# Kernel tuning notes

Hardware: AMD Instinct MI355X
Metric: run time of the kernel (lower is better)

The kernel has to match this reference:

```python
import jax, jax.numpy as jnp
import numpy as np

N = 50000        # nodes
E = 800000       # edges (avg degree 16)
IN_DIM = 256
H = 8            # heads
D = 32           # out_dim per head
T = 4            # edge_type_num
F = 16           # edge_feature_dim
NEG_SLOPE = 0.2


def setup_inputs() -> dict:
    key = jax.random.key(0)
    ks = jax.random.split(key, 9)
    feat = jax.random.normal(ks[0], (N, IN_DIM), dtype=jnp.float32)
    e_pro = jax.random.normal(ks[1], (E, F), dtype=jnp.float32)
    mask = jax.random.uniform(ks[2], (E, T), dtype=jnp.float32)
    W_n = jax.random.normal(ks[3], (IN_DIM, H * D), dtype=jnp.float32) * (1.0 / np.sqrt(IN_DIM))
    attn_l = jax.random.normal(ks[4], (H, D, T), dtype=jnp.float32) * 0.1
    attn_r = jax.random.normal(ks[5], (H, D, T), dtype=jnp.float32) * 0.1
    attn_m = jax.random.normal(ks[6], (H, F, T), dtype=jnp.float32) * 0.1
    src = jax.random.randint(ks[7], (E,), 0, N, dtype=jnp.int32)
    dst = jax.random.randint(ks[8], (E,), 0, N, dtype=jnp.int32)
    return {"feat": feat, "e_pro": e_pro, "mask": mask, "W_n": W_n,
            "attn_l": attn_l, "attn_r": attn_r, "attn_m": attn_m,
            "src": src, "dst": dst}


def reference(feat, e_pro, mask, W_n, attn_l, attn_r, attn_m, src, dst):
    # node projection: [N, H, D]
    feat_src = (feat @ W_n).reshape(N, H, D)

    # per-node attention logits per edge type: [N, H, T]
    el = jnp.einsum("nhd,hdt->nht", feat_src, attn_l)
    er = jnp.einsum("nhd,hdt->nht", feat_src, attn_r)
    # per-edge logits per edge type: [E, H, T]
    em = jnp.einsum("ef,hft->eht", e_pro, attn_m)

    # bmm with edge-type mask [E, T] -> scalar per head: [E, H]
    left = jnp.einsum("eht,et->eh", el[src], mask)
    right = jnp.einsum("eht,et->eh", er[dst], mask)
    em_e = jnp.einsum("eht,et->eh", em, mask)

    e = (left + right + em_e) / 3.0
    e = jnp.where(e > 0, e, NEG_SLOPE * e)  # leaky_relu

    # edge softmax over incoming edges of each dst node (stable)
    e_max = jax.ops.segment_max(e, dst, num_segments=N)          # [N, H]
    e_exp = jnp.exp(e - e_max[dst])                               # [E, H]
    e_sum = jax.ops.segment_sum(e_exp, dst, num_segments=N)      # [N, H]
    a = e_exp / e_sum[dst]                                       # [E, H]

    # u_mul_e + sum aggregation: [E, H, D] -> [N, H, D]
    msg = feat_src[src] * a[:, :, None]
    rst = jax.ops.segment_sum(msg, dst, num_segments=N)

    # cat=True: concat heads
    return rst.reshape(N, H * D)
```

## Files before the change

### kernel.cpp

```cpp
#include <hip/hip_runtime.h>
#include <hip/hip_bf16.h>
#include <hip/hip_fp16.h>

#define NN 50000
#define NEDGE 800000
#define INDIM 256
#define NH 8
#define ND 32
#define HD 256
#define NT 4
#define NF 16

typedef __attribute__((ext_vector_type(8))) short s16x8;
typedef __attribute__((ext_vector_type(4))) float f32x4;
typedef unsigned short u16;

__device__ __forceinline__ float bf2f(u16 u) {
    return __uint_as_float(((unsigned int)u) << 16);
}
__device__ __forceinline__ u16 f2bf(float f) {
    __hip_bfloat16 h = __float2bfloat16(f);
    return *reinterpret_cast<u16*>(&h);
}
__device__ __forceinline__ u16 f2h(float f) {
    __half h = __float2half(f);
    return *reinterpret_cast<u16*>(&h);
}
__device__ __forceinline__ float h2f(u16 u) {
    __half h = *reinterpret_cast<__half*>(&u);
    return __half2float(h);
}

__global__ __launch_bounds__(256) void prep_kernel(const float* __restrict__ W,
                                                   u16* __restrict__ Wt,
                                                   int* __restrict__ cnt,
                                                   int* __restrict__ cursor)
{
    int idx = blockIdx.x * 256 + threadIdx.x;
    int k = idx >> 8, c = idx & 255;
    Wt[(size_t)c * 256 + k] = f2bf(W[idx]);
    if (idx < NN) { cnt[idx] = 0; cursor[idx] = 0; }
}

__global__ __launch_bounds__(256) void gemm_mfma(
    const float* __restrict__ feat, const u16* __restrict__ Wt,
    const int* __restrict__ dst, int* __restrict__ cnt,
    u16* __restrict__ fs, int nrows)
{
    const int tid = threadIdx.x;
    {
        int e0 = (blockIdx.x * 256 + tid) * 2;
        if (e0 < NEDGE)     atomicAdd(&cnt[dst[e0]], 1);
        if (e0 + 1 < NEDGE) atomicAdd(&cnt[dst[e0 + 1]], 1);
    }

    __shared__ u16 At[32 * 256];
    const int brow = blockIdx.x * 32;

    #pragma unroll
    for (int it = 0; it < 4; ++it) {
        int fo = it * 2048 + tid * 8;
        int row = fo >> 8, col = fo & 255;
        int grow = brow + row;
        if (grow >= nrows) grow = nrows - 1;
        const float* gp = feat + (size_t)grow * 256 + col;
        float4 x = *reinterpret_cast<const float4*>(gp);
        float4 y = *reinterpret_cast<const float4*>(gp + 4);
        s16x8 v;
        v[0] = (short)f2bf(x.x); v[1] = (short)f2bf(x.y);
        v[2] = (short)f2bf(x.z); v[3] = (short)f2bf(x.w);
        v[4] = (short)f2bf(y.x); v[5] = (short)f2bf(y.y);
        v[6] = (short)f2bf(y.z); v[7] = (short)f2bf(y.w);
        int byte = (col * 2) ^ ((row & 7) << 4);
        *reinterpret_cast<s16x8*>((char*)At + row * 512 + byte) = v;
    }
    __syncthreads();

    const int wave = tid >> 6, lane = tid & 63;
    const int c0 = wave * 64;
    const int rA = lane & 15;
    const int kg = lane >> 4;

    f32x4 acc[2][4] = {};

    for (int k0 = 0; k0 < 256; k0 += 32) {
        const int kk = k0 + kg * 8;
        const int byte = (kk * 2) ^ ((rA & 7) << 4);
        s16x8 a0 = *reinterpret_cast<const s16x8*>((char*)At + rA * 512 + byte);
        s16x8 a1 = *reinterpret_cast<const s16x8*>((char*)At + (16 + rA) * 512 + byte);
        #pragma unroll
        for (int ct = 0; ct < 4; ++ct) {
            s16x8 b = *reinterpret_cast<const s16x8*>(Wt + (size_t)(c0 + ct * 16 + rA) * 256 + kk);
            acc[0][ct] = __builtin_amdgcn_mfma_f32_16x16x32_bf16(a0, b, acc[0][ct], 0, 0, 0);
            acc[1][ct] = __builtin_amdgcn_mfma_f32_16x16x32_bf16(a1, b, acc[1][ct], 0, 0, 0);
        }
    }

    #pragma unroll
    for (int rt = 0; rt < 2; ++rt) {
        #pragma unroll
        for (int r = 0; r < 4; ++r) {
            int row = brow + rt * 16 + kg * 4 + r;
            if (row < nrows) {
                #pragma unroll
                for (int ct = 0; ct < 4; ++ct) {
                    fs[(size_t)row * 256 + c0 + ct * 16 + rA] = f2bf(acc[rt][ct][r]);
                }
            }
        }
    }
}

__global__ __launch_bounds__(256) void elr_kernel(
    const u16* __restrict__ fs,
    const float* __restrict__ attn_l, const float* __restrict__ attn_r,
    u16* __restrict__ el, u16* __restrict__ er, int n)
{
    __shared__ float s_al[NH * ND * NT];
    __shared__ float s_ar[NH * ND * NT];
    for (int i = threadIdx.x; i < NH * ND * NT; i += 256) {
        s_al[i] = attn_l[i];
        s_ar[i] = attn_r[i];
    }
    __syncthreads();
    int wv = threadIdx.x >> 6, lane = threadIdx.x & 63;
    int node = blockIdx.x * 4 + wv;
    if (node >= n) return;
    int h = lane >> 3, j0 = (lane & 7) * 4;
    ushort4 u = *reinterpret_cast<const ushort4*>(fs + (size_t)node * HD + lane * 4);
    float f0 = bf2f(u.x), f1 = bf2f(u.y), f2 = bf2f(u.z), f3 = bf2f(u.w);
    const float* al = s_al + h * (ND * NT) + j0 * NT;
    const float* ar = s_ar + h * (ND * NT) + j0 * NT;
    float pl[NT], pr[NT];
    #pragma unroll
    for (int t = 0; t < NT; ++t) {
        pl[t] = f0*al[t] + f1*al[NT + t] + f2*al[2*NT + t] + f3*al[3*NT + t];
        pr[t] = f0*ar[t] + f1*ar[NT + t] + f2*ar[2*NT + t] + f3*ar[3*NT + t];
    }
    #pragma unroll
    for (int d = 1; d < 8; d <<= 1) {
        #pragma unroll
        for (int t = 0; t < NT; ++t) {
            pl[t] += __shfl_xor(pl[t], d);
            pr[t] += __shfl_xor(pr[t], d);
        }
    }
    if ((lane & 7) == 0) {
        ushort4 ol, orr;
        ol.x = f2h(pl[0]); ol.y = f2h(pl[1]); ol.z = f2h(pl[2]); ol.w = f2h(pl[3]);
        orr.x = f2h(pr[0]); orr.y = f2h(pr[1]); orr.z = f2h(pr[2]); orr.w = f2h(pr[3]);
        *reinterpret_cast<ushort4*>(el + (size_t)node * (NH*NT) + h * NT) = ol;
        *reinterpret_cast<ushort4*>(er + (size_t)node * (NH*NT) + h * NT) = orr;
    }
}

__global__ void scan1_kernel(const int* __restrict__ cnt, int* __restrict__ off,
                             int* __restrict__ blksum, int n) {
    __shared__ int sm[256];
    int i = blockIdx.x * 256 + threadIdx.x;
    int v = (i < n) ? cnt[i] : 0;
    sm[threadIdx.x] = v;
    __syncthreads();
    for (int d = 1; d < 256; d <<= 1) {
        int t = (threadIdx.x >= d) ? sm[threadIdx.x - d] : 0;
        __syncthreads();
        sm[threadIdx.x] += t;
        __syncthreads();
    }
    if (i < n) off[i] = sm[threadIdx.x] - v;
    if (threadIdx.x == 255) blksum[blockIdx.x] = sm[255];
}

__global__ void scan2_kernel(int* blksum, int nb) {
    __shared__ int sm[256];
    int v = (threadIdx.x < nb) ? blksum[threadIdx.x] : 0;
    sm[threadIdx.x] = v;
    __syncthreads();
    for (int d = 1; d < 256; d <<= 1) {
        int t = (threadIdx.x >= d) ? sm[threadIdx.x - d] : 0;
        __syncthreads();
        sm[threadIdx.x] += t;
        __syncthreads();
    }
    blksum[threadIdx.x] = sm[threadIdx.x] - v;
}

__global__ void scan3_kernel(int* __restrict__ off, const int* __restrict__ blksum,
                             int n, int ne) {
    int i = blockIdx.x * 256 + threadIdx.x;
    if (i < n) off[i] += blksum[blockIdx.x];
    if (i == 0) off[n] = ne;
}

__global__ __launch_bounds__(256) void edge_kernel(
    const float* __restrict__ e_pro, const float* __restrict__ mask,
    const float* __restrict__ attn_m,
    const int* __restrict__ src, const int* __restrict__ dst,
    const u16* __restrict__ el, const u16* __restrict__ er,
    const int* __restrict__ off, int* __restrict__ cursor,
    int2* __restrict__ es, u16* __restrict__ ev, int ne)
{
    __shared__ float4 s_am4[NF][NH];
    __shared__ float s_ep[32][17];
    __shared__ float s_mk[32][5];
    const int tid = threadIdx.x;
    const int eb = blockIdx.x * 32;
    const int j = tid & 7;
    const int el_ = (tid >> 3) & 31;
    const int e = eb + (tid >> 3);

    int s = src[e], d = dst[e];
    int slot = 0;
    if (j == 0) slot = off[d] + atomicAdd(&cursor[d], 1);

    union { uint2 v; u16 u[4]; } lv, rv;
    lv.v = *reinterpret_cast<const uint2*>(el + (size_t)s * (NH*NT) + j * NT);
    rv.v = *reinterpret_cast<const uint2*>(er + (size_t)d * (NH*NT) + j * NT);

    for (int i = tid; i < NH * NF; i += 256) {
        int h = i >> 4, f = i & 15;
        const float* p = attn_m + (size_t)h * (NF * NT) + f * NT;
        s_am4[f][h] = make_float4(p[0], p[1], p[2], p[3]);
    }
    {
        int f2i = tid * 2;
        float2 v = *reinterpret_cast<const float2*>(e_pro + (size_t)eb * NF + f2i);
        int e_l = f2i >> 4, f = f2i & 15;
        s_ep[e_l][f] = v.x; s_ep[e_l][f + 1] = v.y;
    }
    if (tid < 128) {
        s_mk[tid >> 2][tid & 3] = mask[(size_t)eb * NT + tid];
    }
    __syncthreads();

    float4 mk = make_float4(s_mk[el_][0], s_mk[el_][1], s_mk[el_][2], s_mk[el_][3]);

    float em = 0.f;
    #pragma unroll
    for (int f = 0; f < NF; ++f) {
        float4 am = s_am4[f][j];
        float amm = mk.x*am.x + mk.y*am.y + mk.z*am.z + mk.w*am.w;
        em = fmaf(s_ep[el_][f], amm, em);
    }
    float left  = mk.x*h2f(lv.u[0]) + mk.y*h2f(lv.u[1]) + mk.z*h2f(lv.u[2]) + mk.w*h2f(lv.u[3]);
    float right = mk.x*h2f(rv.u[0]) + mk.y*h2f(rv.u[1]) + mk.z*h2f(rv.u[2]) + mk.w*h2f(rv.u[3]);

    float v = (left + right + em) * (1.0f / 3.0f);
    v = v > 0.f ? v : 0.2f * v;
    ev[(size_t)e * NH + j] = f2h(__expf(v));

    if (j == 0) es[slot] = make_int2(e, s);
}

__global__ __launch_bounds__(256) void agg_kernel(
    const int* __restrict__ off, const int2* __restrict__ es,
    const u16* __restrict__ ev, const u16* __restrict__ fs,
    float* __restrict__ out, int n)
{
    int wv = threadIdx.x >> 6, lane = threadIdx.x & 63;
    int node = blockIdx.x * 4 + wv;
    if (node >= n) return;
    int beg = off[node], end = off[node + 1];
    int deg = end - beg;

    int h = lane & 7, sub = lane >> 3;
    float vc[8];
    int sc[8];
    #pragma unroll
    for (int slot = 0; slot < 8; ++slot) {
        int i = beg + slot * 8 + sub;
        float v = 0.f; int sn = 0;
        if (i < end) {
            int2 p = es[i];
            v = h2f(ev[(size_t)p.x * NH + h]);
            sn = p.y;
        }
        vc[slot] = v; sc[slot] = sn;
    }

    int h2 = lane >> 3;
    const int col = lane * 4;
    float a0 = 0.f, a1 = 0.f, a2 = 0.f, a3 = 0.f, sw = 0.f;
    int deg_ = deg < 64 ? deg : 64;
    int nchunk = (deg_ + 7) >> 3;
    #pragma unroll
    for (int c = 0; c < 8; ++c) {
        if (c >= nchunk) break;
        float w8 = vc[c];
        int s8 = sc[c];
        float w[8]; int sn[8];
        #pragma unroll
        for (int q = 0; q < 8; ++q) {
            w[q]  = __shfl(w8, q * 8 + h2);
            sn[q] = __shfl(s8, q * 8 + h2);
        }
        ushort4 u[8];
        #pragma unroll
        for (int q = 0; q < 8; ++q)
            u[q] = *reinterpret_cast<const ushort4*>(fs + (size_t)sn[q] * HD + col);
        #pragma unroll
        for (int q = 0; q < 8; ++q) {
            sw += w[q];
            a0 = fmaf(w[q], bf2f(u[q].x), a0);
            a1 = fmaf(w[q], bf2f(u[q].y), a1);
            a2 = fmaf(w[q], bf2f(u[q].z), a2);
            a3 = fmaf(w[q], bf2f(u[q].w), a3);
        }
    }
    for (int i = beg + 64; i < end; ++i) {
        int2 p = es[i];
        float w = h2f(ev[(size_t)p.x * NH + h2]);
        sw += w;
        ushort4 u = *reinterpret_cast<const ushort4*>(fs + (size_t)p.y * HD + col);
        a0 = fmaf(w, bf2f(u.x), a0); a1 = fmaf(w, bf2f(u.y), a1);
        a2 = fmaf(w, bf2f(u.z), a2); a3 = fmaf(w, bf2f(u.w), a3);
    }
    float invS = sw > 0.f ? 1.f / sw : 0.f;
    a0 *= invS; a1 *= invS; a2 *= invS; a3 *= invS;
    *reinterpret_cast<float4*>(&out[(size_t)node * HD + col]) = make_float4(a0, a1, a2, a3);
}

extern "C" void kernel_launch(void* const* d_in, const int* in_sizes, int n_in,
                              void* d_out, int out_size, void* d_ws, size_t ws_size,
                              hipStream_t stream)
{
    const float* feat   = (const float*)d_in[0];
    const float* e_pro  = (const float*)d_in[1];
    const float* mask   = (const float*)d_in[2];
    const float* W_n    = (const float*)d_in[3];
    const float* attn_l = (const float*)d_in[4];
    const float* attn_r = (const float*)d_in[5];
    const float* attn_m = (const float*)d_in[6];
    const int* src      = (const int*)d_in[7];
    const int* dst      = (const int*)d_in[8];
    float* out = (float*)d_out;

    char* ws = (char*)d_ws;
    size_t o = 0;
    auto alloc = [&](size_t bytes) -> void* {
        void* p = (void*)(ws + o);
        o += (bytes + 255) & ~(size_t)255;
        return p;
    };
    u16* fs     = (u16*)alloc((size_t)NN * HD * 2);
    u16* Wt     = (u16*)alloc((size_t)INDIM * HD * 2);
    u16* el     = (u16*)alloc((size_t)NN * NH * NT * 2);
    u16* er     = (u16*)alloc((size_t)NN * NH * NT * 2);
    u16* ev     = (u16*)alloc((size_t)NEDGE * NH * 2);
    int2* es    = (int2*)alloc((size_t)NEDGE * 8);
    int* cnt    = (int*)alloc((size_t)NN * 4);
    int* cursor = (int*)alloc((size_t)NN * 4);
    int* offs   = (int*)alloc((size_t)(NN + 1) * 4);
    int* blksum = (int*)alloc(256 * 4);
    (void)ws_size; (void)in_sizes; (void)n_in; (void)out_size;

    dim3 b256(256);
    hipLaunchKernelGGL(prep_kernel, dim3(256), b256, 0, stream, W_n, Wt, cnt, cursor);
    hipLaunchKernelGGL(gemm_mfma, dim3((NN + 31) / 32), b256, 0, stream, feat, Wt, dst, cnt, fs, NN);
    hipLaunchKernelGGL(elr_kernel, dim3((NN + 3) / 4), b256, 0, stream, fs, attn_l, attn_r, el, er, NN);
    hipLaunchKernelGGL(scan1_kernel, dim3((NN + 255) / 256), b256, 0, stream, cnt, offs, blksum, NN);
    hipLaunchKernelGGL(scan2_kernel, dim3(1), b256, 0, stream, blksum, (NN + 255) / 256);
    hipLaunchKernelGGL(scan3_kernel, dim3((NN + 255) / 256), b256, 0, stream, offs, blksum, NN, NEDGE);
    hipLaunchKernelGGL(edge_kernel, dim3(NEDGE / 32), b256, 0, stream,
                       e_pro, mask, attn_m, src, dst, el, er, offs, cursor, es, ev, NEDGE);
    hipLaunchKernelGGL(agg_kernel, dim3((NN + 3) / 4), b256, 0, stream,
                       offs, es, ev, fs, out, NN);
}
```

Baseline: 232.0 us.

## Fuse edge logit computation into aggregation kernel, pack mask into CSR entries

Removes the separate edge_kernel. A light fill kernel now scatters the edge id, source and fp16-packed mask into a 16-byte CSR entry, and the aggregation kernel computes the attention logits per edge inline from e_pro, el and the per-node er. This drops the ev intermediate write and read and one wide launch. In exchange the CSR entries are twice as large, e_pro is gathered randomly (64B per edge) inside agg, and each edge's 16-feature dot product is computed in agg, which adds register pressure.

```diff
diff --git a/kernel.cpp b/kernel.cpp
--- a/kernel.cpp
+++ b/kernel.cpp
@@ -192,71 +192,35 @@
     if (i == 0) off[n] = ne;
 }
 
-__global__ __launch_bounds__(256) void edge_kernel(
-    const float* __restrict__ e_pro, const float* __restrict__ mask,
-    const float* __restrict__ attn_m,
-    const int* __restrict__ src, const int* __restrict__ dst,
-    const u16* __restrict__ el, const u16* __restrict__ er,
-    const int* __restrict__ off, int* __restrict__ cursor,
-    int2* __restrict__ es, u16* __restrict__ ev, int ne)
+__global__ void fillidx_kernel(const int* __restrict__ dst, const int* __restrict__ src,
+                               const float* __restrict__ mask,
+                               const int* __restrict__ off, int* __restrict__ cursor,
+                               int4* __restrict__ es, int ne) {
+    int e = blockIdx.x * 256 + threadIdx.x;
+    if (e >= ne) return;
+    int d = dst[e];
+    int s = src[e];
+    float4 mk = *reinterpret_cast<const float4*>(mask + (size_t)e * NT);
+    int pk01 = (int)f2h(mk.x) | ((int)f2h(mk.y) << 16);
+    int pk23 = (int)f2h(mk.z) | ((int)f2h(mk.w) << 16);
+    int slot = off[d] + atomicAdd(&cursor[d], 1);
+    es[slot] = make_int4(e, s, pk01, pk23);
+}
+
+__global__ __launch_bounds__(256) void agg_kernel(
+    const int* __restrict__ off, const int4* __restrict__ es,
+    const float* __restrict__ e_pro, const u16* __restrict__ el,
+    const u16* __restrict__ er, const float* __restrict__ attn_m,
+    const u16* __restrict__ fs, float* __restrict__ out, int n)
 {
     __shared__ float4 s_am4[NF][NH];
-    __shared__ float s_ep[32][17];
-    __shared__ float s_mk[32][5];
-    const int tid = threadIdx.x;
-    const int eb = blockIdx.x * 32;
-    const int j = tid & 7;
-    const int el_ = (tid >> 3) & 31;
-    const int e = eb + (tid >> 3);
-
-    int s = src[e], d = dst[e];
-    int slot = 0;
-    if (j == 0) slot = off[d] + atomicAdd(&cursor[d], 1);
-
-    union { uint2 v; u16 u[4]; } lv, rv;
-    lv.v = *reinterpret_cast<const uint2*>(el + (size_t)s * (NH*NT) + j * NT);
-    rv.v = *reinterpret_cast<const uint2*>(er + (size_t)d * (NH*NT) + j * NT);
-
-    for (int i = tid; i < NH * NF; i += 256) {
-        int h = i >> 4, f = i & 15;
-        const float* p = attn_m + (size_t)h * (NF * NT) + f * NT;
-        s_am4[f][h] = make_float4(p[0], p[1], p[2], p[3]);
-    }
-    {
-        int f2i = tid * 2;
-        float2 v = *reinterpret_cast<const float2*>(e_pro + (size_t)eb * NF + f2i);
-        int e_l = f2i >> 4, f = f2i & 15;
-        s_ep[e_l][f] = v.x; s_ep[e_l][f + 1] = v.y;
-    }
-    if (tid < 128) {
-        s_mk[tid >> 2][tid & 3] = mask[(size_t)eb * NT + tid];
-    }
-    __syncthreads();
-
-    float4 mk = make_float4(s_mk[el_][0], s_mk[el_][1], s_mk[el_][2], s_mk[el_][3]);
-
-    float em = 0.f;
-    #pragma unroll
-    for (int f = 0; f < NF; ++f) {
-        float4 am = s_am4[f][j];
-        float amm = mk.x*am.x + mk.y*am.y + mk.z*am.z + mk.w*am.w;
-        em = fmaf(s_ep[el_][f], amm, em);
-    }
-    float left  = mk.x*h2f(lv.u[0]) + mk.y*h2f(lv.u[1]) + mk.z*h2f(lv.u[2]) + mk.w*h2f(lv.u[3]);
-    float right = mk.x*h2f(rv.u[0]) + mk.y*h2f(rv.u[1]) + mk.z*h2f(rv.u[2]) + mk.w*h2f(rv.u[3]);
-
-    float v = (left + right + em) * (1.0f / 3.0f);
-    v = v > 0.f ? v : 0.2f * v;
-    ev[(size_t)e * NH + j] = f2h(__expf(v));
-
-    if (j == 0) es[slot] = make_int2(e, s);
-}
-
-__global__ __launch_bounds__(256) void agg_kernel(
-    const int* __restrict__ off, const int2* __restrict__ es,
-    const u16* __restrict__ ev, const u16* __restrict__ fs,
-    float* __restrict__ out, int n)
-{
+    for (int i = threadIdx.x; i < NH * NF; i += 256) {
+        int hh = i >> 4, f = i & 15;
+        const float* p = attn_m + (size_t)hh * (NF * NT) + f * NT;
+        s_am4[f][hh] = make_float4(p[0], p[1], p[2], p[3]);
+    }
+    __syncthreads();
+
     int wv = threadIdx.x >> 6, lane = threadIdx.x & 63;
     int node = blockIdx.x * 4 + wv;
     if (node >= n) return;
@@ -264,21 +228,53 @@
     int deg = end - beg;
 
     int h = lane & 7, sub = lane >> 3;
+    int h2 = lane >> 3;
+
+    union { uint2 v; u16 u[4]; } erh, erh2;
+    erh.v  = *reinterpret_cast<const uint2*>(er + (size_t)node * (NH*NT) + h * NT);
+    erh2.v = *reinterpret_cast<const uint2*>(er + (size_t)node * (NH*NT) + h2 * NT);
+    float er0 = h2f(erh.u[0]), er1 = h2f(erh.u[1]), er2 = h2f(erh.u[2]), er3 = h2f(erh.u[3]);
+
+    int4 p[8];
+    #pragma unroll
+    for (int slot = 0; slot < 8; ++slot) {
+        int i = beg + slot * 8 + sub;
+        p[slot] = (i < end) ? es[i] : make_int4(0, 0, 0, 0);
+    }
+
     float vc[8];
     int sc[8];
     #pragma unroll
     for (int slot = 0; slot < 8; ++slot) {
         int i = beg + slot * 8 + sub;
-        float v = 0.f; int sn = 0;
-        if (i < end) {
-            int2 p = es[i];
-            v = h2f(ev[(size_t)p.x * NH + h]);
-            sn = p.y;
-        }
-        vc[slot] = v; sc[slot] = sn;
-    }
-
-    int h2 = lane >> 3;
+        int e = p[slot].x, s = p[slot].y;
+        float mk0 = h2f((u16)(p[slot].z & 0xffff)), mk1 = h2f((u16)((unsigned)p[slot].z >> 16));
+        float mk2 = h2f((u16)(p[slot].w & 0xffff)), mk3 = h2f((u16)((unsigned)p[slot].w >> 16));
+        const float* ep = e_pro + (size_t)e * NF;
+        float4 ep0 = *reinterpret_cast<const float4*>(ep);
+        float4 ep1 = *reinterpret_cast<const float4*>(ep + 4);
+        float4 ep2 = *reinterpret_cast<const float4*>(ep + 8);
+        float4 ep3 = *reinterpret_cast<const float4*>(ep + 12);
+        union { uint2 v; u16 u[4]; } lv;
+        lv.v = *reinterpret_cast<const uint2*>(el + (size_t)s * (NH*NT) + h * NT);
+        float epf[16] = {ep0.x, ep0.y, ep0.z, ep0.w, ep1.x, ep1.y, ep1.z, ep1.w,
+                         ep2.x, ep2.y, ep2.z, ep2.w, ep3.x, ep3.y, ep3.z, ep3.w};
+        float em = 0.f;
+        #pragma unroll
+        for (int f = 0; f < NF; ++f) {
+            float4 am = s_am4[f][h];
+            float amm = mk0*am.x + mk1*am.y + mk2*am.z + mk3*am.w;
+            em = fmaf(epf[f], amm, em);
+        }
+        float left  = mk0*h2f(lv.u[0]) + mk1*h2f(lv.u[1]) + mk2*h2f(lv.u[2]) + mk3*h2f(lv.u[3]);
+        float right = mk0*er0 + mk1*er1 + mk2*er2 + mk3*er3;
+        float v = (left + right + em) * (1.0f / 3.0f);
+        v = v > 0.f ? v : 0.2f * v;
+        float w = __expf(v);
+        vc[slot] = (i < end) ? w : 0.f;
+        sc[slot] = s;
+    }
+
     const int col = lane * 4;
     float a0 = 0.f, a1 = 0.f, a2 = 0.f, a3 = 0.f, sw = 0.f;
     int deg_ = deg < 64 ? deg : 64;
@@ -307,11 +303,28 @@
             a3 = fmaf(w[q], bf2f(u[q].w), a3);
         }
     }
+    float er20 = h2f(erh2.u[0]), er21 = h2f(erh2.u[1]), er22 = h2f(erh2.u[2]), er23 = h2f(erh2.u[3]);
     for (int i = beg + 64; i < end; ++i) {
-        int2 p = es[i];
-        float w = h2f(ev[(size_t)p.x * NH + h2]);
+        int4 q = es[i];
+        float mk0 = h2f((u16)(q.z & 0xffff)), mk1 = h2f((u16)((unsigned)q.z >> 16));
+        float mk2 = h2f((u16)(q.w & 0xffff)), mk3 = h2f((u16)((unsigned)q.w >> 16));
+        const float* ep = e_pro + (size_t)q.x * NF;
+        float em = 0.f;
+        #pragma unroll
+        for (int f = 0; f < NF; ++f) {
+            float4 am = s_am4[f][h2];
+            float amm = mk0*am.x + mk1*am.y + mk2*am.z + mk3*am.w;
+            em = fmaf(ep[f], amm, em);
+        }
+        union { uint2 v; u16 u[4]; } lv;
+        lv.v = *reinterpret_cast<const uint2*>(el + (size_t)q.y * (NH*NT) + h2 * NT);
+        float left  = mk0*h2f(lv.u[0]) + mk1*h2f(lv.u[1]) + mk2*h2f(lv.u[2]) + mk3*h2f(lv.u[3]);
+        float right = mk0*er20 + mk1*er21 + mk2*er22 + mk3*er23;
+        float v = (left + right + em) * (1.0f / 3.0f);
+        v = v > 0.f ? v : 0.2f * v;
+        float w = __expf(v);
         sw += w;
-        ushort4 u = *reinterpret_cast<const ushort4*>(fs + (size_t)p.y * HD + col);
+        ushort4 u = *reinterpret_cast<const ushort4*>(fs + (size_t)q.y * HD + col);
         a0 = fmaf(w, bf2f(u.x), a0); a1 = fmaf(w, bf2f(u.y), a1);
         a2 = fmaf(w, bf2f(u.z), a2); a3 = fmaf(w, bf2f(u.w), a3);
     }
@@ -346,8 +359,7 @@
     u16* Wt     = (u16*)alloc((size_t)INDIM * HD * 2);
     u16* el     = (u16*)alloc((size_t)NN * NH * NT * 2);
     u16* er     = (u16*)alloc((size_t)NN * NH * NT * 2);
-    u16* ev     = (u16*)alloc((size_t)NEDGE * NH * 2);
-    int2* es    = (int2*)alloc((size_t)NEDGE * 8);
+    int4* es    = (int4*)alloc((size_t)NEDGE * 16);
     int* cnt    = (int*)alloc((size_t)NN * 4);
     int* cursor = (int*)alloc((size_t)NN * 4);
     int* offs   = (int*)alloc((size_t)(NN + 1) * 4);
@@ -361,8 +373,8 @@
     hipLaunchKernelGGL(scan1_kernel, dim3((NN + 255) / 256), b256, 0, stream, cnt, offs, blksum, NN);
     hipLaunchKernelGGL(scan2_kernel, dim3(1), b256, 0, stream, blksum, (NN + 255) / 256);
     hipLaunchKernelGGL(scan3_kernel, dim3((NN + 255) / 256), b256, 0, stream, offs, blksum, NN, NEDGE);
-    hipLaunchKernelGGL(edge_kernel, dim3(NEDGE / 32), b256, 0, stream,
-                       e_pro, mask, attn_m, src, dst, el, er, offs, cursor, es, ev, NEDGE);
+    hipLaunchKernelGGL(fillidx_kernel, dim3((NEDGE + 255) / 256), b256, 0, stream,
+                       dst, src, mask, offs, cursor, es, NEDGE);
     hipLaunchKernelGGL(agg_kernel, dim3((NN + 3) / 4), b256, 0, stream,
-                       offs, es, ev, fs, out, NN);
-}
+                       offs, es, e_pro, el, er, attn_m, fs, out, NN);
+}
```

Result: slower. 392.2 us (+69.1%).
